# Kernel optimization log

Hardware: AMD Instinct MI355X
Metric: run time of the kernel (lower is better)

## Reference

```python
import jax, jax.numpy as jnp
import numpy as np

NUM_HEADS = 16
HEAD_DIM = 64
LORA_SCALE = 1.0 / 8.0  # lora_alpha (1) / r (8), loralib defaults


def setup_inputs() -> dict:
    key = jax.random.key(0)
    ks = jax.random.split(key, 10)
    B, N, C = 4, 2048, 1024
    O = 3 * NUM_HEADS * HEAD_DIM  # 3072
    s = lambda fan: 1.0 / np.sqrt(fan)
    return {
        "x": jax.random.normal(ks[0], (B, N, C), jnp.float32),
        "W_qkv": jax.random.normal(ks[1], (O, C), jnp.float32) * s(C),
        "W_lora": jax.random.normal(ks[2], (O, C), jnp.float32) * s(C),
        "b_lora": jax.random.normal(ks[3], (O,), jnp.float32) * s(C),
        "A_q": jax.random.normal(ks[4], (8, C), jnp.float32) * s(C),
        "B_q": jnp.zeros((NUM_HEADS * HEAD_DIM, 8), jnp.float32) + jax.random.normal(ks[5], (NUM_HEADS * HEAD_DIM, 8), jnp.float32) * 0.02,
        "A_v": jax.random.normal(ks[6], (8, C), jnp.float32) * s(C),
        "B_v": jax.random.normal(ks[7], (NUM_HEADS * HEAD_DIM, 8), jnp.float32) * 0.02,
        "W_out": jax.random.normal(ks[8], (C, NUM_HEADS * HEAD_DIM), jnp.float32) * s(NUM_HEADS * HEAD_DIM),
        "b_out": jax.random.normal(ks[9], (C,), jnp.float32) * s(NUM_HEADS * HEAD_DIM),
    }


def reference(x, W_qkv, W_lora, b_lora, A_q, B_q, A_v, B_v, W_out, b_out):
    B, N, C = x.shape
    H, D = NUM_HEADS, HEAD_DIM
    scale = D ** (-0.5)

    def split_qkv(t):
        t = t.reshape(B, N, 3, H, D).transpose(2, 0, 3, 1, 4)
        return t[0], t[1], t[2]

    q, k, v = split_qkv(jnp.einsum('bnc,oc->bno', x, W_qkv))
    ql, _, vl = split_qkv(jnp.einsum('bnc,oc->bno', x, W_lora) + b_lora)

    # low-rank LoRA updates for Q and V slices only (K disabled)
    dq = (jnp.einsum('bnc,rc->bnr', x, A_q) @ B_q.T) * LORA_SCALE  # (B,N,HD)
    dv = (jnp.einsum('bnc,rc->bnr', x, A_v) @ B_v.T) * LORA_SCALE
    dq = dq.reshape(B, N, H, D).transpose(0, 2, 1, 3)
    dv = dv.reshape(B, N, H, D).transpose(0, 2, 1, 3)

    q = q + ql + dq
    v = v + vl + dv

    attn = jax.nn.softmax(jnp.einsum('bhnd,bhmd->bhnm', q, k) * scale, axis=-1)
    out = jnp.einsum('bhnm,bhmd->bhnd', attn, v)
    out = out.transpose(0, 2, 1, 3).reshape(B, N, H * D)  # b h n d -> b n (h d)
    return jnp.einsum('bnk,ck->bnc', out, W_out) + b_out
```

## Files before the change

### kernel.cpp

```cpp
#include <hip/hip_runtime.h>
#include <hip/hip_bf16.h>

typedef unsigned short u16;
typedef unsigned int u32;
typedef __attribute__((ext_vector_type(8))) short bf16x8;
typedef __attribute__((ext_vector_type(4))) float f32x4;
typedef __attribute__((ext_vector_type(16))) float f32x16;

#define GLDS16(gptr, lptr)                                                        \
  __builtin_amdgcn_global_load_lds(                                               \
      (__attribute__((address_space(1))) const void*)(gptr),                      \
      (__attribute__((address_space(3))) void*)(lptr), 16, 0, 0)

__device__ __forceinline__ u16 f2bf(float f) {
  union { float f; unsigned u; } v; v.f = f;
  unsigned r = v.u + 0x7fffu + ((v.u >> 16) & 1u);
  return (u16)(r >> 16);
}

__device__ __forceinline__ u32 pack_bf2(float a, float b) {
  union { __hip_bfloat162 h2; u32 u; } v;
  v.h2 = __float22bfloat162_rn(make_float2(a, b));
  return v.u;
}

__global__ void k_f32_to_bf16(const float* __restrict__ in, u16* __restrict__ out, int n4) {
  int i = blockIdx.x * 256 + threadIdx.x;
  if (i < n4) {
    float4 f = reinterpret_cast<const float4*>(in)[i];
    ushort4 u;
    u.x = f2bf(f.x); u.y = f2bf(f.y); u.z = f2bf(f.z); u.w = f2bf(f.w);
    reinterpret_cast<ushort4*>(out)[i] = u;
  }
}

__global__ void k_prep_weff(const float* __restrict__ Wqkv, const float* __restrict__ Wlora,
                            const float* __restrict__ blora,
                            const float* __restrict__ Aq, const float* __restrict__ Bq,
                            const float* __restrict__ Av, const float* __restrict__ Bv,
                            u16* __restrict__ Weff, float* __restrict__ beff) {
  int idx = blockIdx.x * 256 + threadIdx.x;
  int o = idx >> 10, c = idx & 1023;
  float w = Wqkv[idx];
  if (o < 1024) {
    float lr = 0.f;
#pragma unroll
    for (int r = 0; r < 8; ++r) lr += Bq[o * 8 + r] * Aq[r * 1024 + c];
    w += Wlora[idx] + 0.125f * lr;
  } else if (o >= 2048) {
    int o2 = o - 2048;
    float lr = 0.f;
#pragma unroll
    for (int r = 0; r < 8; ++r) lr += Bv[o2 * 8 + r] * Av[r * 1024 + c];
    w += Wlora[idx] + 0.125f * lr;
  }
  Weff[idx] = f2bf(w);
  if (c == 0) beff[o] = (o < 1024 || o >= 2048) ? blora[o] : 0.f;
}

__global__ __launch_bounds__(256, 2)
void k_gemm_qkv(const u16* __restrict__ Xb, const u16* __restrict__ Weff,
                const float* __restrict__ beff, u16* __restrict__ Y) {
  __shared__ u16 As[128 * 32], Bs[128 * 32];
  const int tid = threadIdx.x, lane = tid & 63, wave = tid >> 6;
  const int lr = lane & 15, lg = lane >> 4;
  const int wr = wave >> 1, wc = wave & 1;
  const int m0 = blockIdx.y * 128, n0 = blockIdx.x * 128;
  f32x4 acc[4][4] = {};

  for (int k0 = 0; k0 < 1024; k0 += 32) {
#pragma unroll
    for (int i = 0; i < 2; ++i) {
      int gc = ((tid & 3) ^ ((tid >> 2) & 3)) << 3;
      GLDS16(Xb + (size_t)(m0 + i * 64 + (tid >> 2)) * 1024 + k0 + gc, As + i * 2048 + wave * 512);
      GLDS16(Weff + (size_t)(n0 + i * 64 + (tid >> 2)) * 1024 + k0 + gc, Bs + i * 2048 + wave * 512);
    }
    __syncthreads();
    bf16x8 af[4], bfr[4];
#pragma unroll
    for (int t = 0; t < 4; ++t) {
      int ch = ((lg ^ (lr & 3)) & 3) << 3;
      af[t]  = *reinterpret_cast<const bf16x8*>(As + (wr * 64 + t * 16 + lr) * 32 + ch);
      bfr[t] = *reinterpret_cast<const bf16x8*>(Bs + (wc * 64 + t * 16 + lr) * 32 + ch);
    }
#pragma unroll
    for (int mi = 0; mi < 4; ++mi)
#pragma unroll
      for (int ni = 0; ni < 4; ++ni)
        acc[mi][ni] = __builtin_amdgcn_mfma_f32_16x16x32_bf16(af[mi], bfr[ni], acc[mi][ni], 0, 0, 0);
    __syncthreads();
  }

#pragma unroll
  for (int mi = 0; mi < 4; ++mi) {
    int row = m0 + wr * 64 + mi * 16 + (lg << 2);
#pragma unroll
    for (int ni = 0; ni < 4; ++ni) {
      int col = n0 + wc * 64 + ni * 16 + lr;
      float bias = beff[col];
#pragma unroll
      for (int j = 0; j < 4; ++j) {
        float v = acc[mi][ni][j] + bias;
        if (col < 1024) v *= 0.18033688011112042f;
        Y[(size_t)(row + j) * 3072 + col] = f2bf(v);
      }
    }
  }
}

__global__ __launch_bounds__(256)
void k_vtrans(const u16* __restrict__ Y, u16* __restrict__ Vt) {
  __shared__ u16 Ls[64 * 65];
  const int t = threadIdx.x;
  const int bh = blockIdx.y, b = bh >> 4, h = bh & 15;
  const int n0 = blockIdx.x * 64;
#pragma unroll
  for (int c = 0; c < 2; ++c) {
    int idx = c * 256 + t;
    int nl = idx >> 3, d0 = (idx & 7) * 8;
    bf16x8 val = *reinterpret_cast<const bf16x8*>(
        Y + (size_t)(b * 2048 + n0 + nl) * 3072 + 2048 + h * 64 + d0);
#pragma unroll
    for (int j = 0; j < 8; ++j) Ls[(d0 + j) * 65 + nl] = (u16)val[j];
  }
  __syncthreads();
#pragma unroll
  for (int c = 0; c < 2; ++c) {
    int idx = c * 256 + t;
    int dl = idx >> 3, nn = (idx & 7) * 8;
    bf16x8 outv;
#pragma unroll
    for (int j = 0; j < 8; ++j) outv[j] = (short)Ls[dl * 65 + nn + j];
    *reinterpret_cast<bf16x8*>(Vt + (size_t)(bh * 64 + dl) * 2048 + n0 + nn) = outv;
  }
}

__global__ __launch_bounds__(256, 3)
void k_attn(const u16* __restrict__ Y, const u16* __restrict__ Vt, u16* __restrict__ Oa) {
  __shared__ u16 Ks[2][64 * 64], Vs[2][64 * 64];
  const int tid = threadIdx.x, lane = tid & 63, wave = tid >> 6;
  const int b = blockIdx.y >> 4, h = blockIdx.y & 15;
  const int q0 = blockIdx.x * 128;
  const int l31 = lane & 31, hi = lane >> 5;
  const size_t bq = (size_t)b * 2048;
  const size_t bv = (size_t)b * 1024 + h * 64;
  const int hc = h * 64;

  bf16x8 qb[4];
  {
    const u16* yr = Y + (bq + q0 + wave * 32 + l31) * 3072 + hc + hi * 8;
#pragma unroll
    for (int ks = 0; ks < 4; ++ks)
      qb[ks] = *reinterpret_cast<const bf16x8*>(yr + ks * 16);
  }

  float m_run = -1e30f, l_run = 0.f;
  f32x16 oacc[2] = {};

  const int sr = tid >> 3, sc = tid & 7;
  auto stage = [&](int key0, int bb) {
#pragma unroll
    for (int i = 0; i < 2; ++i) {
      int r = i * 32 + sr;
      int gc = (sc ^ (r & 7)) << 3;
      GLDS16(Y + (bq + key0 + r) * 3072 + 1024 + hc + gc, &Ks[bb][i * 2048 + wave * 512]);
      GLDS16(Vt + (bv + r) * 2048 + key0 + gc,            &Vs[bb][i * 2048 + wave * 512]);
    }
  };

  stage(0, 0);
  for (int kt = 0; kt < 32; ++kt) {
    const int cur = kt & 1;
    if (kt < 31) {
      stage((kt + 1) * 64, cur ^ 1);
      asm volatile("s_waitcnt vmcnt(4)" ::: "memory");
    } else {
      asm volatile("s_waitcnt vmcnt(0)" ::: "memory");
    }
    __builtin_amdgcn_s_barrier();
    asm volatile("" ::: "memory");

    bf16x8 kb[2][4], vb[2][4];
#pragma unroll
    for (int t = 0; t < 2; ++t) {
      const u16* kbase = &Ks[cur][(t * 32 + l31) * 64];
      int rx = (t * 32 + l31) & 7;
#pragma unroll
      for (int ks = 0; ks < 4; ++ks)
        kb[t][ks] = *reinterpret_cast<const bf16x8*>(kbase + (((ks * 2 + hi) ^ rx) << 3));
    }
#pragma unroll
    for (int dt = 0; dt < 2; ++dt) {
      const u16* vbase = &Vs[cur][(dt * 32 + l31) * 64];
      int rx = (dt * 32 + l31) & 7;
#pragma unroll
      for (int ks = 0; ks < 4; ++ks)
        vb[dt][ks] = *reinterpret_cast<const bf16x8*>(vbase + (((ks * 2 + hi) ^ rx) << 3));
    }

    f32x16 p4[2] = {};
    __builtin_amdgcn_s_setprio(1);
#pragma unroll
    for (int t = 0; t < 2; ++t)
#pragma unroll
      for (int ks = 0; ks < 4; ++ks)
        p4[t] = __builtin_amdgcn_mfma_f32_32x32x16_bf16(kb[t][ks], qb[ks], p4[t], 0, 0, 0);
    __builtin_amdgcn_s_setprio(0);

    float mx[8];
#pragma unroll
    for (int r = 0; r < 8; ++r)
      mx[r] = fmaxf(fmaxf(p4[0][r], p4[0][r + 8]), fmaxf(p4[1][r], p4[1][r + 8]));
#pragma unroll
    for (int s = 4; s > 0; s >>= 1)
#pragma unroll
      for (int r = 0; r < s; ++r) mx[r] = fmaxf(mx[r], mx[r + s]);
    float tmax = fmaxf(mx[0], __shfl_xor(mx[0], 32));

    if (__any(tmax > m_run + 11.0f)) {
      float mnew = fmaxf(m_run, tmax);
      float alpha = __builtin_amdgcn_exp2f(m_run - mnew);
      m_run = mnew;
      l_run *= alpha;
#pragma unroll
      for (int r = 0; r < 16; ++r) {
        float ab = __shfl(alpha, (r & 3) + 8 * (r >> 2) + 4 * hi);
        oacc[0][r] *= ab;
        oacc[1][r] *= ab;
      }
    }

    float rs = 0.f;
    u32 w[2][4][2];
#pragma unroll
    for (int t = 0; t < 2; ++t)
#pragma unroll
      for (int g = 0; g < 4; ++g) {
        float e0 = __builtin_amdgcn_exp2f(p4[t][4 * g + 0] - m_run);
        float e1 = __builtin_amdgcn_exp2f(p4[t][4 * g + 1] - m_run);
        float e2 = __builtin_amdgcn_exp2f(p4[t][4 * g + 2] - m_run);
        float e3 = __builtin_amdgcn_exp2f(p4[t][4 * g + 3] - m_run);
        rs += (e0 + e1) + (e2 + e3);
        w[t][g][0] = pack_bf2(e0, e1);
        w[t][g][1] = pack_bf2(e2, e3);
      }
    rs += __shfl_xor(rs, 32);
    l_run += rs;

    bf16x8 pa[4];
#pragma unroll
    for (int ks = 0; ks < 4; ++ks) {
      const int t = ks >> 1, q2 = (ks & 1) * 2;
      auto s0 = __builtin_amdgcn_permlane32_swap(w[t][q2][0], w[t][q2 + 1][0], false, false);
      auto s1 = __builtin_amdgcn_permlane32_swap(w[t][q2][1], w[t][q2 + 1][1], false, false);
      union { u32 u[4]; bf16x8 v; } cv;
      cv.u[0] = s0[0]; cv.u[1] = s1[0]; cv.u[2] = s0[1]; cv.u[3] = s1[1];
      pa[ks] = cv.v;
    }

    __builtin_amdgcn_s_setprio(1);
#pragma unroll
    for (int ks = 0; ks < 4; ++ks) {
      oacc[0] = __builtin_amdgcn_mfma_f32_32x32x16_bf16(pa[ks], vb[0][ks], oacc[0], 0, 0, 0);
      oacc[1] = __builtin_amdgcn_mfma_f32_32x32x16_bf16(pa[ks], vb[1][ks], oacc[1], 0, 0, 0);
    }
    __builtin_amdgcn_s_setprio(0);

    asm volatile("" ::: "memory");
    __builtin_amdgcn_s_barrier();
  }

  float linv = __builtin_amdgcn_rcpf(l_run);
  const size_t orow0 = bq + q0 + wave * 32;
#pragma unroll
  for (int r = 0; r < 16; ++r) {
    int qr = (r & 3) + 8 * (r >> 2) + 4 * hi;
    float li = __shfl(linv, qr);
    size_t rb = (orow0 + qr) * 1024 + hc + l31;
    Oa[rb]      = f2bf(oacc[0][r] * li);
    Oa[rb + 32] = f2bf(oacc[1][r] * li);
  }
}

__global__ __launch_bounds__(256, 2)
void k_gemm_out(const u16* __restrict__ Ob, const u16* __restrict__ Wb,
                const float* __restrict__ bout, float* __restrict__ out) {
  __shared__ u16 As[128 * 32], Bs[128 * 32];
  const int tid = threadIdx.x, lane = tid & 63, wave = tid >> 6;
  const int lr = lane & 15, lg = lane >> 4;
  const int wr = wave >> 1, wc = wave & 1;
  const int m0 = blockIdx.y * 128, n0 = blockIdx.x * 128;
  f32x4 acc[4][4] = {};

  for (int k0 = 0; k0 < 1024; k0 += 32) {
#pragma unroll
    for (int i = 0; i < 2; ++i) {
      int gc = ((tid & 3) ^ ((tid >> 2) & 3)) << 3;
      GLDS16(Ob + (size_t)(m0 + i * 64 + (tid >> 2)) * 1024 + k0 + gc, As + i * 2048 + wave * 512);
      GLDS16(Wb + (size_t)(n0 + i * 64 + (tid >> 2)) * 1024 + k0 + gc, Bs + i * 2048 + wave * 512);
    }
    __syncthreads();
    bf16x8 af[4], bfr[4];
#pragma unroll
    for (int t = 0; t < 4; ++t) {
      int ch = ((lg ^ (lr & 3)) & 3) << 3;
      af[t]  = *reinterpret_cast<const bf16x8*>(As + (wr * 64 + t * 16 + lr) * 32 + ch);
      bfr[t] = *reinterpret_cast<const bf16x8*>(Bs + (wc * 64 + t * 16 + lr) * 32 + ch);
    }
#pragma unroll
    for (int mi = 0; mi < 4; ++mi)
#pragma unroll
      for (int ni = 0; ni < 4; ++ni)
        acc[mi][ni] = __builtin_amdgcn_mfma_f32_16x16x32_bf16(af[mi], bfr[ni], acc[mi][ni], 0, 0, 0);
    __syncthreads();
  }

#pragma unroll
  for (int mi = 0; mi < 4; ++mi) {
    int row = m0 + wr * 64 + mi * 16 + (lg << 2);
#pragma unroll
    for (int ni = 0; ni < 4; ++ni) {
      int col = n0 + wc * 64 + ni * 16 + lr;
      float bias = bout[col];
#pragma unroll
      for (int j = 0; j < 4; ++j)
        out[(size_t)(row + j) * 1024 + col] = acc[mi][ni][j] + bias;
    }
  }
}

extern "C" void kernel_launch(void* const* d_in, const int* in_sizes, int n_in,
                              void* d_out, int out_size, void* d_ws, size_t ws_size,
                              hipStream_t stream) {
  const float* x     = (const float*)d_in[0];
  const float* Wqkv  = (const float*)d_in[1];
  const float* Wlora = (const float*)d_in[2];
  const float* blora = (const float*)d_in[3];
  const float* Aq    = (const float*)d_in[4];
  const float* Bq    = (const float*)d_in[5];
  const float* Av    = (const float*)d_in[6];
  const float* Bv    = (const float*)d_in[7];
  const float* Wout  = (const float*)d_in[8];
  const float* bout  = (const float*)d_in[9];
  float* out = (float*)d_out;

  char* w = (char*)d_ws;
  auto alloc = [&](size_t bytes) { char* p = w; w += (bytes + 255) & ~(size_t)255; return p; };
  u16*   Xb    = (u16*)alloc((size_t)8192 * 1024 * 2);
  u16*   Weff  = (u16*)alloc((size_t)3072 * 1024 * 2);
  float* beff  = (float*)alloc((size_t)3072 * 4);
  u16*   Woutb = (u16*)alloc((size_t)1024 * 1024 * 2);
  u16*   Y     = (u16*)alloc((size_t)8192 * 3072 * 2);
  u16*   Vt    = (u16*)alloc((size_t)4096 * 1024 * 2 * 2);
  u16*   Oa    = Xb;

  k_f32_to_bf16<<<dim3(8192), dim3(256), 0, stream>>>(x, Xb, 8192 * 1024 / 4);
  k_f32_to_bf16<<<dim3(1024), dim3(256), 0, stream>>>(Wout, Woutb, 1024 * 1024 / 4);
  k_prep_weff<<<dim3(12288), dim3(256), 0, stream>>>(Wqkv, Wlora, blora, Aq, Bq, Av, Bv, Weff, beff);
  k_gemm_qkv<<<dim3(24, 64), dim3(256), 0, stream>>>(Xb, Weff, beff, Y);
  k_vtrans<<<dim3(32, 64), dim3(256), 0, stream>>>(Y, Vt);
  k_attn<<<dim3(16, 64), dim3(256), 0, stream>>>(Y, Vt, Oa);
  k_gemm_out<<<dim3(8, 64), dim3(256), 0, stream>>>(Oa, Woutb, bout, out);
}
```

Before: 335.5 us.

## Fuse prep kernels, swizzle GEMM tile order, unroll attention loop, raise occupancy

Merges the three prep launches (x cast, W_out cast, effective QKV weight build) into one kernel indexed by block range, removing two launches. Both GEMMs remap workgroup IDs with an XCD-style swizzle so neighbouring tiles share operands in cache. The attention key loop is unrolled by two with fixed LDS buffers, its row-max reduction is rewritten as a linear chain, and launch bounds are raised on the GEMMs and attention to allow more resident blocks. Higher occupancy bounds may force register spills.

```diff
diff --git a/kernel.cpp b/kernel.cpp
--- a/kernel.cpp
+++ b/kernel.cpp
@@ -24,48 +24,57 @@
   return v.u;
 }
 
-__global__ void k_f32_to_bf16(const float* __restrict__ in, u16* __restrict__ out, int n4) {
-  int i = blockIdx.x * 256 + threadIdx.x;
-  if (i < n4) {
-    float4 f = reinterpret_cast<const float4*>(in)[i];
+__global__ void k_prep(const float* __restrict__ x, const float* __restrict__ Wqkv,
+                       const float* __restrict__ Wlora, const float* __restrict__ blora,
+                       const float* __restrict__ Aq, const float* __restrict__ Bq,
+                       const float* __restrict__ Av, const float* __restrict__ Bv,
+                       const float* __restrict__ Wout,
+                       u16* __restrict__ Xb, u16* __restrict__ Weff,
+                       float* __restrict__ beff, u16* __restrict__ Woutb) {
+  const int bid = blockIdx.x, tid = threadIdx.x;
+  if (bid < 8192) {
+    int i = bid * 256 + tid;
+    float4 f = reinterpret_cast<const float4*>(x)[i];
     ushort4 u;
     u.x = f2bf(f.x); u.y = f2bf(f.y); u.z = f2bf(f.z); u.w = f2bf(f.w);
-    reinterpret_cast<ushort4*>(out)[i] = u;
-  }
-}
-
-__global__ void k_prep_weff(const float* __restrict__ Wqkv, const float* __restrict__ Wlora,
-                            const float* __restrict__ blora,
-                            const float* __restrict__ Aq, const float* __restrict__ Bq,
-                            const float* __restrict__ Av, const float* __restrict__ Bv,
-                            u16* __restrict__ Weff, float* __restrict__ beff) {
-  int idx = blockIdx.x * 256 + threadIdx.x;
-  int o = idx >> 10, c = idx & 1023;
-  float w = Wqkv[idx];
-  if (o < 1024) {
-    float lr = 0.f;
-#pragma unroll
-    for (int r = 0; r < 8; ++r) lr += Bq[o * 8 + r] * Aq[r * 1024 + c];
-    w += Wlora[idx] + 0.125f * lr;
-  } else if (o >= 2048) {
-    int o2 = o - 2048;
-    float lr = 0.f;
-#pragma unroll
-    for (int r = 0; r < 8; ++r) lr += Bv[o2 * 8 + r] * Av[r * 1024 + c];
-    w += Wlora[idx] + 0.125f * lr;
-  }
-  Weff[idx] = f2bf(w);
-  if (c == 0) beff[o] = (o < 1024 || o >= 2048) ? blora[o] : 0.f;
-}
-
-__global__ __launch_bounds__(256, 2)
+    reinterpret_cast<ushort4*>(Xb)[i] = u;
+  } else if (bid < 9216) {
+    int i = (bid - 8192) * 256 + tid;
+    float4 f = reinterpret_cast<const float4*>(Wout)[i];
+    ushort4 u;
+    u.x = f2bf(f.x); u.y = f2bf(f.y); u.z = f2bf(f.z); u.w = f2bf(f.w);
+    reinterpret_cast<ushort4*>(Woutb)[i] = u;
+  } else {
+    int idx = (bid - 9216) * 256 + tid;
+    int o = idx >> 10, c = idx & 1023;
+    float w = Wqkv[idx];
+    if (o < 1024) {
+      float lr = 0.f;
+#pragma unroll
+      for (int r = 0; r < 8; ++r) lr += Bq[o * 8 + r] * Aq[r * 1024 + c];
+      w += Wlora[idx] + 0.125f * lr;
+    } else if (o >= 2048) {
+      int o2 = o - 2048;
+      float lr = 0.f;
+#pragma unroll
+      for (int r = 0; r < 8; ++r) lr += Bv[o2 * 8 + r] * Av[r * 1024 + c];
+      w += Wlora[idx] + 0.125f * lr;
+    }
+    Weff[idx] = f2bf(w);
+    if (c == 0) beff[o] = (o < 1024 || o >= 2048) ? blora[o] : 0.f;
+  }
+}
+
+__global__ __launch_bounds__(256, 3)
 void k_gemm_qkv(const u16* __restrict__ Xb, const u16* __restrict__ Weff,
                 const float* __restrict__ beff, u16* __restrict__ Y) {
   __shared__ u16 As[128 * 32], Bs[128 * 32];
   const int tid = threadIdx.x, lane = tid & 63, wave = tid >> 6;
   const int lr = lane & 15, lg = lane >> 4;
   const int wr = wave >> 1, wc = wave & 1;
-  const int m0 = blockIdx.y * 128, n0 = blockIdx.x * 128;
+  const int wg = blockIdx.x + 24 * blockIdx.y;
+  const int swz = (wg & 7) * 192 + (wg >> 3);
+  const int m0 = (swz / 24) * 128, n0 = (swz % 24) * 128;
   f32x4 acc[4][4] = {};
 
   for (int k0 = 0; k0 < 1024; k0 += 32) {
@@ -135,7 +144,7 @@
   }
 }
 
-__global__ __launch_bounds__(256, 3)
+__global__ __launch_bounds__(256, 4)
 void k_attn(const u16* __restrict__ Y, const u16* __restrict__ Vt, u16* __restrict__ Oa) {
   __shared__ u16 Ks[2][64 * 64], Vs[2][64 * 64];
   const int tid = threadIdx.x, lane = tid & 63, wave = tid >> 6;
@@ -168,22 +177,11 @@
     }
   };
 
-  stage(0, 0);
-  for (int kt = 0; kt < 32; ++kt) {
-    const int cur = kt & 1;
-    if (kt < 31) {
-      stage((kt + 1) * 64, cur ^ 1);
-      asm volatile("s_waitcnt vmcnt(4)" ::: "memory");
-    } else {
-      asm volatile("s_waitcnt vmcnt(0)" ::: "memory");
-    }
-    __builtin_amdgcn_s_barrier();
-    asm volatile("" ::: "memory");
-
+  auto compute = [&](const u16* __restrict__ Kt, const u16* __restrict__ Vti) {
     bf16x8 kb[2][4], vb[2][4];
 #pragma unroll
     for (int t = 0; t < 2; ++t) {
-      const u16* kbase = &Ks[cur][(t * 32 + l31) * 64];
+      const u16* kbase = Kt + (t * 32 + l31) * 64;
       int rx = (t * 32 + l31) & 7;
 #pragma unroll
       for (int ks = 0; ks < 4; ++ks)
@@ -191,7 +189,7 @@
     }
 #pragma unroll
     for (int dt = 0; dt < 2; ++dt) {
-      const u16* vbase = &Vs[cur][(dt * 32 + l31) * 64];
+      const u16* vbase = Vti + (dt * 32 + l31) * 64;
       int rx = (dt * 32 + l31) & 7;
 #pragma unroll
       for (int ks = 0; ks < 4; ++ks)
@@ -207,15 +205,12 @@
         p4[t] = __builtin_amdgcn_mfma_f32_32x32x16_bf16(kb[t][ks], qb[ks], p4[t], 0, 0, 0);
     __builtin_amdgcn_s_setprio(0);
 
-    float mx[8];
-#pragma unroll
-    for (int r = 0; r < 8; ++r)
-      mx[r] = fmaxf(fmaxf(p4[0][r], p4[0][r + 8]), fmaxf(p4[1][r], p4[1][r + 8]));
-#pragma unroll
-    for (int s = 4; s > 0; s >>= 1)
-#pragma unroll
-      for (int r = 0; r < s; ++r) mx[r] = fmaxf(mx[r], mx[r + s]);
-    float tmax = fmaxf(mx[0], __shfl_xor(mx[0], 32));
+    float tmax = fmaxf(p4[0][0], p4[0][1]);
+#pragma unroll
+    for (int r = 2; r < 16; r += 2) tmax = fmaxf(fmaxf(tmax, p4[0][r]), p4[0][r + 1]);
+#pragma unroll
+    for (int r = 0; r < 16; r += 2) tmax = fmaxf(fmaxf(tmax, p4[1][r]), p4[1][r + 1]);
+    tmax = fmaxf(tmax, __shfl_xor(tmax, 32));
 
     if (__any(tmax > m_run + 11.0f)) {
       float mnew = fmaxf(m_run, tmax);
@@ -265,7 +260,26 @@
       oacc[1] = __builtin_amdgcn_mfma_f32_32x32x16_bf16(pa[ks], vb[1][ks], oacc[1], 0, 0, 0);
     }
     __builtin_amdgcn_s_setprio(0);
-
+  };
+
+  stage(0, 0);
+  for (int kt = 0; kt < 32; kt += 2) {
+    stage((kt + 1) * 64, 1);
+    asm volatile("s_waitcnt vmcnt(4)" ::: "memory");
+    __builtin_amdgcn_s_barrier();
+    asm volatile("" ::: "memory");
+    compute(Ks[0], Vs[0]);
+    asm volatile("" ::: "memory");
+    __builtin_amdgcn_s_barrier();
+    if (kt + 2 < 32) {
+      stage((kt + 2) * 64, 0);
+      asm volatile("s_waitcnt vmcnt(4)" ::: "memory");
+    } else {
+      asm volatile("s_waitcnt vmcnt(0)" ::: "memory");
+    }
+    __builtin_amdgcn_s_barrier();
+    asm volatile("" ::: "memory");
+    compute(Ks[1], Vs[1]);
     asm volatile("" ::: "memory");
     __builtin_amdgcn_s_barrier();
   }
@@ -282,14 +296,16 @@
   }
 }
 
-__global__ __launch_bounds__(256, 2)
+__global__ __launch_bounds__(256, 3)
 void k_gemm_out(const u16* __restrict__ Ob, const u16* __restrict__ Wb,
                 const float* __restrict__ bout, float* __restrict__ out) {
   __shared__ u16 As[128 * 32], Bs[128 * 32];
   const int tid = threadIdx.x, lane = tid & 63, wave = tid >> 6;
   const int lr = lane & 15, lg = lane >> 4;
   const int wr = wave >> 1, wc = wave & 1;
-  const int m0 = blockIdx.y * 128, n0 = blockIdx.x * 128;
+  const int wg = blockIdx.x + 8 * blockIdx.y;
+  const int swz = (wg & 7) * 64 + (wg >> 3);
+  const int m0 = (swz >> 3) * 128, n0 = (swz & 7) * 128;
   f32x4 acc[4][4] = {};
 
   for (int k0 = 0; k0 < 1024; k0 += 32) {
@@ -354,9 +370,8 @@
   u16*   Vt    = (u16*)alloc((size_t)4096 * 1024 * 2 * 2);
   u16*   Oa    = Xb;
 
-  k_f32_to_bf16<<<dim3(8192), dim3(256), 0, stream>>>(x, Xb, 8192 * 1024 / 4);
-  k_f32_to_bf16<<<dim3(1024), dim3(256), 0, stream>>>(Wout, Woutb, 1024 * 1024 / 4);
-  k_prep_weff<<<dim3(12288), dim3(256), 0, stream>>>(Wqkv, Wlora, blora, Aq, Bq, Av, Bv, Weff, beff);
+  k_prep<<<dim3(21504), dim3(256), 0, stream>>>(x, Wqkv, Wlora, blora, Aq, Bq, Av, Bv, Wout,
+                                                Xb, Weff, beff, Woutb);
   k_gemm_qkv<<<dim3(24, 64), dim3(256), 0, stream>>>(Xb, Weff, beff, Y);
   k_vtrans<<<dim3(32, 64), dim3(256), 0, stream>>>(Y, Vt);
   k_attn<<<dim3(16, 64), dim3(256), 0, stream>>>(Y, Vt, Oa);
```

Result: slower. 437.4 us (+30.4%).
